# Kernel tuning notes

Measured on AMD Instinct MI355X. Metric: run time of the kernel, lower is better.

The kernel has to match this reference:

```python
import jax, jax.numpy as jnp
import numpy as np

D_MODEL = 1024
NUM_HEADS = 16
D_K = D_MODEL // NUM_HEADS


def setup_inputs() -> dict:
    key = jax.random.key(0)
    ks = jax.random.split(key, 9)
    s = 1.0 / np.sqrt(D_MODEL)
    return {
        "z": jax.random.normal(ks[0], (4, 2048, D_MODEL), dtype=jnp.float32),
        "Wq": jax.random.uniform(ks[1], (D_MODEL, D_MODEL), jnp.float32, -s, s),
        "bq": jax.random.uniform(ks[2], (D_MODEL,), jnp.float32, -s, s),
        "Wk": jax.random.uniform(ks[3], (D_MODEL, D_MODEL), jnp.float32, -s, s),
        "bk": jax.random.uniform(ks[4], (D_MODEL,), jnp.float32, -s, s),
        "Wv": jax.random.uniform(ks[5], (D_MODEL, D_MODEL), jnp.float32, -s, s),
        "bv": jax.random.uniform(ks[6], (D_MODEL,), jnp.float32, -s, s),
        "Wo": jax.random.uniform(ks[7], (D_MODEL, D_MODEL), jnp.float32, -s, s),
        "bo": jax.random.uniform(ks[8], (D_MODEL,), jnp.float32, -s, s),
    }


def reference(z, Wq, bq, Wk, bk, Wv, bv, Wo, bo):
    B, S, _ = z.shape
    # project and split heads: [B, H, S, d_k]
    def proj(W, b):
        return (z @ W.T + b).reshape(B, S, NUM_HEADS, D_K).transpose(0, 2, 1, 3)
    Q, K, V = proj(Wq, bq), proj(Wk, bk), proj(Wv, bv)
    scale = 1.0 / np.sqrt(D_K)
    scores = jnp.einsum('bhqd,bhkd->bhqk', Q, K) * scale
    probs = jax.nn.softmax(scores, axis=-1)
    ctx = jnp.einsum('bhqk,bhkd->bhqd', probs, V)
    ctx = ctx.transpose(0, 2, 1, 3).reshape(B, S, D_MODEL)
    return ctx @ Wo.T + bo
```

## Files before the change

kernel.cpp:

```cpp
#include <hip/hip_runtime.h>
#include <stdint.h>

#define D_MODEL 1024
#define NHEAD 16
#define DKH 64
#define BATCH 4
#define SEQ 2048
#define M_ROWS (BATCH*SEQ)
#define NBH (BATCH*NHEAD)

typedef float f32x4 __attribute__((ext_vector_type(4)));
typedef float f32x16 __attribute__((ext_vector_type(16)));
typedef __bf16 bf16x8 __attribute__((ext_vector_type(8)));
typedef __bf16 bf16x4v __attribute__((ext_vector_type(4)));
typedef short short4v __attribute__((ext_vector_type(4)));
typedef unsigned int uint2v __attribute__((ext_vector_type(2)));

__device__ __forceinline__ unsigned short f2bf(float x) {
    __bf16 b = (__bf16)x;
    return __builtin_bit_cast(unsigned short, b);
}

#define GLL(gsrc, ldst) \
    __builtin_amdgcn_global_load_lds((const __attribute__((address_space(1))) void*)(gsrc), \
                                     (__attribute__((address_space(3))) void*)(ldst), 16, 0, 0)

__global__ __launch_bounds__(256) void k_convert(
    const float* __restrict__ z,  const float* __restrict__ wq,
    const float* __restrict__ wk, const float* __restrict__ wv,
    const float* __restrict__ wo,
    const float* __restrict__ bq, const float* __restrict__ bk,
    const float* __restrict__ bv,
    unsigned short* __restrict__ zb, unsigned short* __restrict__ wqkv,
    unsigned short* __restrict__ wob, float* __restrict__ biasf)
{
    int i = blockIdx.x * 256 + threadIdx.x;
    {
        float4 v = ((const float4*)z)[i];
        ushort4 o; o.x = f2bf(v.x); o.y = f2bf(v.y); o.z = f2bf(v.z); o.w = f2bf(v.w);
        ((ushort4*)zb)[i] = o;
    }
    if (i < 262144) {
        float4 v;
        ushort4 o;
        v = ((const float4*)wq)[i];
        o.x=f2bf(v.x); o.y=f2bf(v.y); o.z=f2bf(v.z); o.w=f2bf(v.w);
        ((ushort4*)wqkv)[i] = o;
        v = ((const float4*)wk)[i];
        o.x=f2bf(v.x); o.y=f2bf(v.y); o.z=f2bf(v.z); o.w=f2bf(v.w);
        ((ushort4*)wqkv)[262144 + i] = o;
        v = ((const float4*)wv)[i];
        o.x=f2bf(v.x); o.y=f2bf(v.y); o.z=f2bf(v.z); o.w=f2bf(v.w);
        ((ushort4*)wqkv)[524288 + i] = o;
        v = ((const float4*)wo)[i];
        o.x=f2bf(v.x); o.y=f2bf(v.y); o.z=f2bf(v.z); o.w=f2bf(v.w);
        ((ushort4*)wob)[i] = o;
    }
    if (i < 1024) {
        biasf[i]        = bq[i];
        biasf[1024 + i] = bk[i];
        biasf[2048 + i] = bv[i];
    }
}

__global__ __launch_bounds__(256) void k_gemm_qkv(
    const unsigned short* __restrict__ A,
    const unsigned short* __restrict__ Bw,
    const float* __restrict__ biasf,
    unsigned short* __restrict__ qb, unsigned short* __restrict__ kb,
    unsigned short* __restrict__ vtb)
{
    __shared__ unsigned short lds_a[128 * 32];
    __shared__ unsigned short lds_b[128 * 32];

    const int NT = 3072 / 128;
    int bid = blockIdx.x;
    int tn = bid % NT, tm = bid / NT;
    int m0 = tm * 128, n0 = tn * 128;
    int tid = threadIdx.x, wid = tid >> 6, lane = tid & 63;
    int wm = wid >> 1, wn = wid & 1;

    f32x4 acc[4][4] = {};

    int srow = lane >> 2;
    int scol = (lane & 3) * 8;

    for (int kt = 0; kt < 32; ++kt) {
        int k0 = kt * 32;
#pragma unroll
        for (int i = 0; i < 2; ++i) {
            int rb = (wid * 2 + i) * 16;
            GLL(A  + (size_t)(m0 + rb + srow) * 1024 + k0 + scol, lds_a + rb * 32);
            GLL(Bw + (size_t)(n0 + rb + srow) * 1024 + k0 + scol, lds_b + rb * 32);
        }
        __syncthreads();
        bf16x8 af[4], bfr[4];
#pragma unroll
        for (int i = 0; i < 4; ++i)
            af[i] = *(const bf16x8*)(lds_a + (wm * 64 + i * 16 + (lane & 15)) * 32 + (lane >> 4) * 8);
#pragma unroll
        for (int j = 0; j < 4; ++j)
            bfr[j] = *(const bf16x8*)(lds_b + (wn * 64 + j * 16 + (lane & 15)) * 32 + (lane >> 4) * 8);
#pragma unroll
        for (int i = 0; i < 4; ++i)
#pragma unroll
            for (int j = 0; j < 4; ++j)
                acc[i][j] = __builtin_amdgcn_mfma_f32_16x16x32_bf16(af[i], bfr[j], acc[i][j], 0, 0, 0);
        __syncthreads();
    }

    const float QSC = 0.18033688011112042f;
    int t = n0 >> 10;
#pragma unroll
    for (int j = 0; j < 4; ++j) {
        int col = n0 + wn * 64 + j * 16 + (lane & 15);
        float bias = biasf[col];
        int d  = col & 1023;
        int h  = d >> 6;
        int dk = d & 63;
#pragma unroll
        for (int i = 0; i < 4; ++i) {
#pragma unroll
            for (int r = 0; r < 4; ++r) {
                int row = m0 + wm * 64 + i * 16 + (lane >> 4) * 4 + r;
                float v = acc[i][j][r] + bias;
                if (t == 0) v *= QSC;
                unsigned short bv16 = f2bf(v);
                int b_ = row >> 11, s_ = row & 2047;
                int bh = b_ * NHEAD + h;
                if (t == 0)      qb[((size_t)bh * SEQ + s_) * DKH + dk] = bv16;
                else if (t == 1) kb[((size_t)bh * SEQ + s_) * DKH + dk] = bv16;
                else             vtb[((size_t)bh * DKH + dk) * SEQ + s_] = bv16;
            }
        }
    }
}

__device__ __forceinline__ void stage_kv(
    const unsigned short* __restrict__ kb, const unsigned short* __restrict__ vtb,
    unsigned short* lk, unsigned short* lv,
    int bh, int t, int wid, int srow8, int sc)
{
#pragma unroll
    for (int i = 0; i < 2; ++i) {
        int rb = wid * 16 + i * 8;
        int row = rb + srow8;
        int cs = (sc ^ (row & 7)) * 8;
        GLL(kb  + ((size_t)bh * SEQ + t * 64 + row) * DKH + cs, lk + rb * 64);
        GLL(vtb + ((size_t)bh * DKH + row) * SEQ + t * 64 + cs, lv + rb * 64);
    }
}

__global__ __launch_bounds__(256) void k_attn(
    const unsigned short* __restrict__ qg,
    const unsigned short* __restrict__ kb,
    const unsigned short* __restrict__ vtb,
    unsigned short* __restrict__ ctxb)
{
    __shared__ unsigned short lds_k[2][64 * 64];
    __shared__ unsigned short lds_v[2][64 * 64];

    int bid = blockIdx.x;
    int x = bid & 7, li = bid >> 3;
    int bh = x * 8 + (li >> 4);
    int qt = li & 15;

    int tid = threadIdx.x, wid = tid >> 6, lane = tid & 63;
    int lq = lane & 31, hi = lane >> 5;
    int srow8 = lane >> 3, sc = lane & 7;

    bf16x8 aq[4];
    {
        const unsigned short* qp = qg + ((size_t)bh * SEQ + qt * 128 + wid * 32 + lq) * DKH + hi * 8;
#pragma unroll
        for (int d = 0; d < 4; ++d) aq[d] = *(const bf16x8*)(qp + d * 16);
    }

    float lsum = 0.f;
    f32x16 oa0 = {};
    f32x16 oa1 = {};

    stage_kv(kb, vtb, &lds_k[0][0], &lds_v[0][0], bh, 0, wid, srow8, sc);
    asm volatile("s_waitcnt vmcnt(0)" ::: "memory");
    __builtin_amdgcn_s_barrier();

    for (int kt = 0; kt < 32; ++kt) {
        int cur = kt & 1;
        if (kt < 31)
            stage_kv(kb, vtb, &lds_k[cur ^ 1][0], &lds_v[cur ^ 1][0], bh, kt + 1, wid, srow8, sc);

        f32x16 st0 = {}, st1 = {};
        __builtin_amdgcn_s_setprio(1);
#pragma unroll
        for (int ds = 0; ds < 4; ++ds) {
            int ch = ds * 2 + hi;
            bf16x8 kf0 = *(const bf16x8*)(&lds_k[cur][(lq)      * 64 + ((ch ^ (lq & 7)) * 8)]);
            bf16x8 kf1 = *(const bf16x8*)(&lds_k[cur][(32 + lq) * 64 + ((ch ^ (lq & 7)) * 8)]);
            st0 = __builtin_amdgcn_mfma_f32_32x32x16_bf16(kf0, aq[ds], st0, 0, 0, 0);
            st1 = __builtin_amdgcn_mfma_f32_32x32x16_bf16(kf1, aq[ds], st1, 0, 0, 0);
        }
        __builtin_amdgcn_s_setprio(0);

        short4v w[8];
#pragma unroll
        for (int ks = 0; ks < 4; ++ks) {
            {
                float p0 = __builtin_amdgcn_exp2f(st0[4 * ks + 0]);
                float p1 = __builtin_amdgcn_exp2f(st0[4 * ks + 1]);
                float p2 = __builtin_amdgcn_exp2f(st0[4 * ks + 2]);
                float p3 = __builtin_amdgcn_exp2f(st0[4 * ks + 3]);
                lsum += (p0 + p1) + (p2 + p3);
                bf16x4v pb;
                pb[0] = (__bf16)p0; pb[1] = (__bf16)p1; pb[2] = (__bf16)p2; pb[3] = (__bf16)p3;
                w[ks] = __builtin_bit_cast(short4v, pb);
            }
            {
                float p0 = __builtin_amdgcn_exp2f(st1[4 * ks + 0]);
                float p1 = __builtin_amdgcn_exp2f(st1[4 * ks + 1]);
                float p2 = __builtin_amdgcn_exp2f(st1[4 * ks + 2]);
                float p3 = __builtin_amdgcn_exp2f(st1[4 * ks + 3]);
                lsum += (p0 + p1) + (p2 + p3);
                bf16x4v pb;
                pb[0] = (__bf16)p0; pb[1] = (__bf16)p1; pb[2] = (__bf16)p2; pb[3] = (__bf16)p3;
                w[4 + ks] = __builtin_bit_cast(short4v, pb);
            }
        }

        __builtin_amdgcn_s_setprio(1);
#pragma unroll
        for (int ks = 0; ks < 8; ++ks) {
            int co = ((ks ^ (lq & 7)) * 16) + hi * 8;
            short4v vf0 = *(const short4v*)((const char*)&lds_v[cur][(lq)      * 64] + co);
            short4v vf1 = *(const short4v*)((const char*)&lds_v[cur][(32 + lq) * 64] + co);
            oa0 = __builtin_amdgcn_mfma_f32_32x32x8bf16_1k(vf0, w[ks], oa0, 0, 0, 0);
            oa1 = __builtin_amdgcn_mfma_f32_32x32x8bf16_1k(vf1, w[ks], oa1, 0, 0, 0);
        }
        __builtin_amdgcn_s_setprio(0);

        if (kt < 31) {
            asm volatile("s_waitcnt vmcnt(0)" ::: "memory");
            __builtin_amdgcn_sched_barrier(0);
            __builtin_amdgcn_s_barrier();
        }
    }

    int b_ = bh >> 4, h = bh & 15;
    lsum += __shfl_xor(lsum, 32);
    float inv = 1.0f / lsum;
    int s_ = qt * 128 + wid * 32 + lq;
    unsigned short* op = ctxb + (((size_t)b_ * SEQ + s_) * NHEAD + h) * DKH;
#pragma unroll
    for (int m = 0; m < 4; ++m) {
        {
            unsigned int u0 = ((unsigned int)f2bf(oa0[4 * m + 1] * inv) << 16) | f2bf(oa0[4 * m + 0] * inv);
            unsigned int u1 = ((unsigned int)f2bf(oa0[4 * m + 3] * inv) << 16) | f2bf(oa0[4 * m + 2] * inv);
            *(uint2v*)(op + 8 * m + 4 * hi) = (uint2v){ u0, u1 };
        }
        {
            unsigned int u0 = ((unsigned int)f2bf(oa1[4 * m + 1] * inv) << 16) | f2bf(oa1[4 * m + 0] * inv);
            unsigned int u1 = ((unsigned int)f2bf(oa1[4 * m + 3] * inv) << 16) | f2bf(oa1[4 * m + 2] * inv);
            *(uint2v*)(op + 32 + 8 * m + 4 * hi) = (uint2v){ u0, u1 };
        }
    }
}

__global__ __launch_bounds__(256) void k_gemm_out(
    const unsigned short* __restrict__ A,
    const unsigned short* __restrict__ Bw,
    const float* __restrict__ bo,
    float* __restrict__ out)
{
    __shared__ unsigned short lds_a[128 * 32];
    __shared__ unsigned short lds_b[128 * 32];

    const int NT = 1024 / 128;
    int bid = blockIdx.x;
    int tn = bid % NT, tm = bid / NT;
    int m0 = tm * 128, n0 = tn * 128;
    int tid = threadIdx.x, wid = tid >> 6, lane = tid & 63;
    int wm = wid >> 1, wn = wid & 1;

    f32x4 acc[4][4] = {};

    int srow = lane >> 2;
    int scol = (lane & 3) * 8;

    for (int kt = 0; kt < 32; ++kt) {
        int k0 = kt * 32;
#pragma unroll
        for (int i = 0; i < 2; ++i) {
            int rb = (wid * 2 + i) * 16;
            GLL(A  + (size_t)(m0 + rb + srow) * 1024 + k0 + scol, lds_a + rb * 32);
            GLL(Bw + (size_t)(n0 + rb + srow) * 1024 + k0 + scol, lds_b + rb * 32);
        }
        __syncthreads();
        bf16x8 af[4], bfr[4];
#pragma unroll
        for (int i = 0; i < 4; ++i)
            af[i] = *(const bf16x8*)(lds_a + (wm * 64 + i * 16 + (lane & 15)) * 32 + (lane >> 4) * 8);
#pragma unroll
        for (int j = 0; j < 4; ++j)
            bfr[j] = *(const bf16x8*)(lds_b + (wn * 64 + j * 16 + (lane & 15)) * 32 + (lane >> 4) * 8);
#pragma unroll
        for (int i = 0; i < 4; ++i)
#pragma unroll
            for (int j = 0; j < 4; ++j)
                acc[i][j] = __builtin_amdgcn_mfma_f32_16x16x32_bf16(af[i], bfr[j], acc[i][j], 0, 0, 0);
        __syncthreads();
    }

#pragma unroll
    for (int j = 0; j < 4; ++j) {
        int col = n0 + wn * 64 + j * 16 + (lane & 15);
        float bias = bo[col];
#pragma unroll
        for (int i = 0; i < 4; ++i) {
#pragma unroll
            for (int r = 0; r < 4; ++r) {
                int row = m0 + wm * 64 + i * 16 + (lane >> 4) * 4 + r;
                out[(size_t)row * 1024 + col] = acc[i][j][r] + bias;
            }
        }
    }
}

extern "C" void kernel_launch(void* const* d_in, const int* in_sizes, int n_in,
                              void* d_out, int out_size, void* d_ws, size_t ws_size,
                              hipStream_t stream)
{
    const float* z  = (const float*)d_in[0];
    const float* Wq = (const float*)d_in[1];
    const float* bq = (const float*)d_in[2];
    const float* Wk = (const float*)d_in[3];
    const float* bk = (const float*)d_in[4];
    const float* Wv = (const float*)d_in[5];
    const float* bv = (const float*)d_in[6];
    const float* Wo = (const float*)d_in[7];
    const float* bo = (const float*)d_in[8];
    float* out = (float*)d_out;

    char* ws = (char*)d_ws;
    unsigned short* zb   = (unsigned short*)(ws);
    unsigned short* ctxb = (unsigned short*)(ws);
    unsigned short* wqkv = (unsigned short*)(ws + (16ull << 20));
    unsigned short* wob  = (unsigned short*)(ws + (22ull << 20));
    float*          biasf= (float*)(ws + (24ull << 20));
    unsigned short* qb   = (unsigned short*)(ws + (25ull << 20));
    unsigned short* kb   = (unsigned short*)(ws + (41ull << 20));
    unsigned short* vtb  = (unsigned short*)(ws + (57ull << 20));

    k_convert<<<8192, 256, 0, stream>>>(z, Wq, Wk, Wv, Wo, bq, bk, bv, zb, wqkv, wob, biasf);
    k_gemm_qkv<<<64 * 24, 256, 0, stream>>>(zb, wqkv, biasf, qb, kb, vtb);
    k_attn<<<NBH * 16, 256, 0, stream>>>(qb, kb, vtb, ctxb);
    k_gemm_out<<<64 * 8, 256, 0, stream>>>(ctxb, wob, bo, out);
}
```

Before: 239.3 us.

## Pre-swizzle K/V into MFMA fragment order and double attention block size

The QKV GEMM epilogue now writes K and V^T directly in per-64-key tiles laid out in the exact MFMA fragment order. The attention kernel can then stage each tile with one contiguous global-to-LDS load per wave and read fragments with linear lane-indexed LDS reads, with no XOR swizzle arithmetic. Attention blocks grow from 256 to 512 threads (256 queries), so each staged K/V tile is shared by twice as many waves and the grid is halved. The trade-offs are scattered 2-byte stores in the GEMM epilogue, possible LDS bank conflicts on the unswizzled reads, and fewer, larger blocks.

```diff
diff --git a/kernel.cpp b/kernel.cpp
--- a/kernel.cpp
+++ b/kernel.cpp
@@ -128,50 +128,46 @@
                 unsigned short bv16 = f2bf(v);
                 int b_ = row >> 11, s_ = row & 2047;
                 int bh = b_ * NHEAD + h;
-                if (t == 0)      qb[((size_t)bh * SEQ + s_) * DKH + dk] = bv16;
-                else if (t == 1) kb[((size_t)bh * SEQ + s_) * DKH + dk] = bv16;
-                else             vtb[((size_t)bh * DKH + dk) * SEQ + s_] = bv16;
+                if (t == 0) {
+                    qb[((size_t)bh * SEQ + s_) * DKH + dk] = bv16;
+                } else if (t == 1) {
+                    int kvblk = s_ >> 6, r64 = s_ & 63;
+                    int t32 = r64 >> 5, l5 = r64 & 31;
+                    int ds = dk >> 4, hi2 = (dk >> 3) & 1, e = dk & 7;
+                    kb[((size_t)(bh * 32 + kvblk)) * 4096 +
+                       (t32 * 4 + ds) * 512 + (hi2 * 32 + l5) * 8 + e] = bv16;
+                } else {
+                    int kvblk = s_ >> 6, kv64 = s_ & 63;
+                    int ks = kv64 >> 3, hi2 = (kv64 >> 2) & 1, e = kv64 & 3;
+                    int vt = dk >> 5, l5 = dk & 31;
+                    vtb[((size_t)(bh * 32 + kvblk)) * 4096 +
+                        (vt * 8 + ks) * 256 + (hi2 * 32 + l5) * 4 + e] = bv16;
+                }
             }
         }
     }
 }
 
-__device__ __forceinline__ void stage_kv(
-    const unsigned short* __restrict__ kb, const unsigned short* __restrict__ vtb,
-    unsigned short* lk, unsigned short* lv,
-    int bh, int t, int wid, int srow8, int sc)
-{
-#pragma unroll
-    for (int i = 0; i < 2; ++i) {
-        int rb = wid * 16 + i * 8;
-        int row = rb + srow8;
-        int cs = (sc ^ (row & 7)) * 8;
-        GLL(kb  + ((size_t)bh * SEQ + t * 64 + row) * DKH + cs, lk + rb * 64);
-        GLL(vtb + ((size_t)bh * DKH + row) * SEQ + t * 64 + cs, lv + rb * 64);
-    }
-}
-
-__global__ __launch_bounds__(256) void k_attn(
+__global__ __launch_bounds__(512) void k_attn(
     const unsigned short* __restrict__ qg,
     const unsigned short* __restrict__ kb,
     const unsigned short* __restrict__ vtb,
     unsigned short* __restrict__ ctxb)
 {
-    __shared__ unsigned short lds_k[2][64 * 64];
-    __shared__ unsigned short lds_v[2][64 * 64];
+    __shared__ unsigned short lds_k[2][4096];
+    __shared__ unsigned short lds_v[2][4096];
 
     int bid = blockIdx.x;
     int x = bid & 7, li = bid >> 3;
-    int bh = x * 8 + (li >> 4);
-    int qt = li & 15;
+    int bh = x * 8 + (li >> 3);
+    int qt = li & 7;
 
     int tid = threadIdx.x, wid = tid >> 6, lane = tid & 63;
     int lq = lane & 31, hi = lane >> 5;
-    int srow8 = lane >> 3, sc = lane & 7;
 
     bf16x8 aq[4];
     {
-        const unsigned short* qp = qg + ((size_t)bh * SEQ + qt * 128 + wid * 32 + lq) * DKH + hi * 8;
+        const unsigned short* qp = qg + ((size_t)bh * SEQ + qt * 256 + wid * 32 + lq) * DKH + hi * 8;
 #pragma unroll
         for (int d = 0; d < 4; ++d) aq[d] = *(const bf16x8*)(qp + d * 16);
     }
@@ -180,22 +176,28 @@
     f32x16 oa0 = {};
     f32x16 oa1 = {};
 
-    stage_kv(kb, vtb, &lds_k[0][0], &lds_v[0][0], bh, 0, wid, srow8, sc);
+    const unsigned short* kbase = kb  + (size_t)bh * 32 * 4096;
+    const unsigned short* vbase = vtb + (size_t)bh * 32 * 4096;
+    int so = wid * 512 + lane * 8;
+
+    GLL(kbase + so, &lds_k[0][wid * 512]);
+    GLL(vbase + so, &lds_v[0][wid * 512]);
     asm volatile("s_waitcnt vmcnt(0)" ::: "memory");
     __builtin_amdgcn_s_barrier();
 
     for (int kt = 0; kt < 32; ++kt) {
         int cur = kt & 1;
-        if (kt < 31)
-            stage_kv(kb, vtb, &lds_k[cur ^ 1][0], &lds_v[cur ^ 1][0], bh, kt + 1, wid, srow8, sc);
+        if (kt < 31) {
+            GLL(kbase + (size_t)(kt + 1) * 4096 + so, &lds_k[cur ^ 1][wid * 512]);
+            GLL(vbase + (size_t)(kt + 1) * 4096 + so, &lds_v[cur ^ 1][wid * 512]);
+        }
 
         f32x16 st0 = {}, st1 = {};
         __builtin_amdgcn_s_setprio(1);
 #pragma unroll
         for (int ds = 0; ds < 4; ++ds) {
-            int ch = ds * 2 + hi;
-            bf16x8 kf0 = *(const bf16x8*)(&lds_k[cur][(lq)      * 64 + ((ch ^ (lq & 7)) * 8)]);
-            bf16x8 kf1 = *(const bf16x8*)(&lds_k[cur][(32 + lq) * 64 + ((ch ^ (lq & 7)) * 8)]);
+            bf16x8 kf0 = *(const bf16x8*)(&lds_k[cur][(ds)     * 512 + lane * 8]);
+            bf16x8 kf1 = *(const bf16x8*)(&lds_k[cur][(4 + ds) * 512 + lane * 8]);
             st0 = __builtin_amdgcn_mfma_f32_32x32x16_bf16(kf0, aq[ds], st0, 0, 0, 0);
             st1 = __builtin_amdgcn_mfma_f32_32x32x16_bf16(kf1, aq[ds], st1, 0, 0, 0);
         }
@@ -229,9 +231,8 @@
         __builtin_amdgcn_s_setprio(1);
 #pragma unroll
         for (int ks = 0; ks < 8; ++ks) {
-            int co = ((ks ^ (lq & 7)) * 16) + hi * 8;
-            short4v vf0 = *(const short4v*)((const char*)&lds_v[cur][(lq)      * 64] + co);
-            short4v vf1 = *(const short4v*)((const char*)&lds_v[cur][(32 + lq) * 64] + co);
+            short4v vf0 = *(const short4v*)(&lds_v[cur][(ks)     * 256 + lane * 4]);
+            short4v vf1 = *(const short4v*)(&lds_v[cur][(8 + ks) * 256 + lane * 4]);
             oa0 = __builtin_amdgcn_mfma_f32_32x32x8bf16_1k(vf0, w[ks], oa0, 0, 0, 0);
             oa1 = __builtin_amdgcn_mfma_f32_32x32x8bf16_1k(vf1, w[ks], oa1, 0, 0, 0);
         }
@@ -247,7 +248,7 @@
     int b_ = bh >> 4, h = bh & 15;
     lsum += __shfl_xor(lsum, 32);
     float inv = 1.0f / lsum;
-    int s_ = qt * 128 + wid * 32 + lq;
+    int s_ = qt * 256 + wid * 32 + lq;
     unsigned short* op = ctxb + (((size_t)b_ * SEQ + s_) * NHEAD + h) * DKH;
 #pragma unroll
     for (int m = 0; m < 4; ++m) {
@@ -351,6 +352,6 @@
 
     k_convert<<<8192, 256, 0, stream>>>(z, Wq, Wk, Wv, Wo, bq, bk, bv, zb, wqkv, wob, biasf);
     k_gemm_qkv<<<64 * 24, 256, 0, stream>>>(zb, wqkv, biasf, qb, kb, vtb);
-    k_attn<<<NBH * 16, 256, 0, stream>>>(qb, kb, vtb, ctxb);
+    k_attn<<<NBH * 8, 512, 0, stream>>>(qb, kb, vtb, ctxb);
     k_gemm_out<<<64 * 8, 256, 0, stream>>>(ctxb, wob, bo, out);
 }
```

Result: faster. 227.4 us (-5.0%).
